# Kernel tuning notes

Hardware: AMD Instinct MI355X
Metric: run time of the kernel (lower is better)

## Reference

```python
import jax, jax.numpy as jnp
import numpy as np

D_MODEL = 1024
NHEAD = 16
HEAD_DIM = D_MODEL // NHEAD
ROPE_BASE = 10000.0


def rotate_half(x):
    h = x.shape[-1] // 2
    return jnp.concatenate((-x[..., h:], x[..., :h]), axis=-1)


def rope_cos_sin(seq_len, dim, dtype):
    inv_freq = 1.0 / (ROPE_BASE ** (jnp.arange(0, dim, 2, dtype=jnp.float32) / dim))
    t = jnp.arange(seq_len, dtype=jnp.float32)
    freqs = jnp.einsum('i,j->ij', t, inv_freq)  # [S, dim/2]
    emb = jnp.concatenate((freqs, freqs), axis=-1)  # [S, dim]
    return jnp.cos(emb).astype(dtype), jnp.sin(emb).astype(dtype)


def setup_inputs() -> dict:
    key = jax.random.key(0)
    ks = jax.random.split(key, 9)
    b, s = 2, 2048
    lim = 1.0 / np.sqrt(D_MODEL)
    def lin(kw, kb):
        W = jax.random.uniform(kw, (D_MODEL, D_MODEL), jnp.float32, -lim, lim)
        bia = jax.random.uniform(kb, (D_MODEL,), jnp.float32, -lim, lim)
        return W, bia
    Wq, bq = lin(ks[0], ks[1])
    Wk, bk = lin(ks[2], ks[3])
    Wv, bv = lin(ks[4], ks[5])
    Wo, bo = lin(ks[6], ks[7])
    x = jax.random.normal(ks[8], (b, s, D_MODEL), jnp.float32)
    return {"x": x, "Wq": Wq, "bq": bq, "Wk": Wk, "bk": bk,
            "Wv": Wv, "bv": bv, "Wo": Wo, "bo": bo}


def reference(x, Wq, bq, Wk, bk, Wv, bv, Wo, bo):
    b, s, _ = x.shape
    scale = jnp.sqrt(jnp.asarray(HEAD_DIM, x.dtype))
    # projections (torch Linear: y = x @ W.T + b)
    q = x @ Wq.T + bq
    k = x @ Wk.T + bk
    v = x @ Wv.T + bv
    # [b, h, s, d]
    def split_heads(t):
        return t.reshape(b, s, NHEAD, HEAD_DIM).transpose(0, 2, 1, 3)
    q, k, v = split_heads(q), split_heads(k), split_heads(v)
    cos, sin = rope_cos_sin(s, HEAD_DIM, x.dtype)  # [s, d]
    q = q * cos + rotate_half(q) * sin
    k = k * cos + rotate_half(k) * sin
    scores = jnp.einsum('bhqd,bhkd->bhqk', q, k) / scale
    probs = jax.nn.softmax(scores, axis=-1)
    out = jnp.einsum('bhqk,bhkd->bhqd', probs, v)
    out = out.transpose(0, 2, 1, 3).reshape(b, s, D_MODEL)
    return out @ Wo.T + bo
```

## Files before the change

kernel.cpp:

```cpp
#include <hip/hip_runtime.h>
#include <hip/hip_bf16.h>
#include <stdint.h>


typedef __attribute__((ext_vector_type(8))) short bf16x8;
typedef __attribute__((ext_vector_type(4))) float f32x4;
typedef __attribute__((ext_vector_type(16))) float f32x16;
typedef __attribute__((ext_vector_type(4))) short short4v;
typedef __attribute__((ext_vector_type(4))) float float4v;
typedef __attribute__((ext_vector_type(4))) unsigned uint32x4;

#define DEV __device__ __forceinline__

DEV short f2bf(float f) {
  union { float f; uint32_t u; } v; v.f = f;
  uint32_t r = (v.u + 0x7fffu + ((v.u >> 16) & 1u)) >> 16;
  return (short)(uint16_t)r;
}
DEV float bf2f(short b) {
  union { uint32_t u; float f; } v; v.u = ((uint32_t)(uint16_t)b) << 16;
  return v.f;
}
DEV unsigned cvtpk(float a, float b) {
  unsigned d;
  asm("v_cvt_pk_bf16_f32 %0, %1, %2" : "=v"(d) : "v"(a), "v"(b));
  return d;
}
DEV void gload16(const void* g, const void* l) {
  __builtin_amdgcn_global_load_lds((const __attribute__((address_space(1))) void*)g,
                                   (__attribute__((address_space(3))) void*)l, 16, 0, 0);
}

__global__ void convert_kernel(const float* __restrict__ x,
                               const float* __restrict__ wq, const float* __restrict__ wk,
                               const float* __restrict__ wv, const float* __restrict__ wo,
                               short* __restrict__ xb, short* __restrict__ wqb,
                               short* __restrict__ wkb, short* __restrict__ wvb,
                               short* __restrict__ wob,
                               float* __restrict__ ct, float* __restrict__ st) {
  const int idx = blockIdx.x * blockDim.x + threadIdx.x;
  if (idx >= 2097152) {
    const int i2 = idx - 2097152;
    const int t = i2 >> 5, j = i2 & 31;
    const float f = (float)t * exp2f(-(float)j * (13.287712379549449f / 32.f));
    ct[i2] = cosf(f);
    st[i2] = sinf(f);
    return;
  }
  const float* src; short* dst; int off;
  if (idx < 1048576)      { src = x;  dst = xb;  off = idx; }
  else if (idx < 1310720) { src = wq; dst = wqb; off = idx - 1048576; }
  else if (idx < 1572864) { src = wk; dst = wkb; off = idx - 1310720; }
  else if (idx < 1835008) { src = wv; dst = wvb; off = idx - 1572864; }
  else                    { src = wo; dst = wob; off = idx - 1835008; }
  float4v v = *(const float4v*)(src + (size_t)off * 4);
  short4v o;
  o[0] = f2bf(v[0]); o[1] = f2bf(v[1]); o[2] = f2bf(v[2]); o[3] = f2bf(v[3]);
  *(short4v*)(dst + (size_t)off * 4) = o;
}

template<bool FINAL>
__global__ __launch_bounds__(256, 2) void gemm_bt(
    const short* __restrict__ A,
    const short* __restrict__ W0, const short* __restrict__ W1, const short* __restrict__ W2,
    const float* __restrict__ b0, const float* __restrict__ b1, const float* __restrict__ b2,
    short* __restrict__ o0, short* __restrict__ o1, short* __restrict__ o2,
    float* __restrict__ of,
    const float* __restrict__ ct, const float* __restrict__ st) {
  constexpr int K = 1024;
  __shared__ short lds[2 * 128 * 64];
  short* As = lds;
  short* Ws = lds + 128 * 64;

  const int tid = threadIdx.x;
  const int lane = tid & 63;
  const int w = tid >> 6;
  const int wr = w >> 1, wc = w & 1;
  const int bn = blockIdx.x, bm = blockIdx.y, z = blockIdx.z;

  const short* Wt = (z == 0) ? W0 : (z == 1 ? W1 : W2);
  const float* bias = (z == 0) ? b0 : (z == 1 ? b1 : b2);
  short* ob = (z == 0) ? o0 : (z == 1 ? o1 : o2);

  const int lrow = lane >> 3;
  const int clog = 16 * ((lane & 7) ^ lrow);

  f32x4 acc[4][4] = {};
  const size_t arowbase = (size_t)(bm * 128) * K;
  const size_t wrowbase = (size_t)(bn * 128) * K;

  for (int kt = 0; kt < K / 64; ++kt) {
    __syncthreads();
#pragma unroll
    for (int i = 0; i < 4; ++i) {
      const int c = i * 4 + w;
      const int row = c * 8 + lrow;
      gload16(A + arowbase + (size_t)row * K + kt * 64 + (clog >> 1),
              (const char*)As + c * 1024);
      gload16(Wt + wrowbase + (size_t)row * K + kt * 64 + (clog >> 1),
              (const char*)Ws + c * 1024);
    }
    __syncthreads();
#pragma unroll
    for (int kk = 0; kk < 2; ++kk) {
      bf16x8 af[4], bf[4];
      const int kb = (kk * 32 + (lane >> 4) * 8) * 2;
#pragma unroll
      for (int mi = 0; mi < 4; ++mi) {
        const int row = wr * 64 + mi * 16 + (lane & 15);
        af[mi] = *(const bf16x8*)((const char*)As + row * 128 + (kb ^ ((row & 7) << 4)));
      }
#pragma unroll
      for (int ni = 0; ni < 4; ++ni) {
        const int row = wc * 64 + ni * 16 + (lane & 15);
        bf[ni] = *(const bf16x8*)((const char*)Ws + row * 128 + (kb ^ ((row & 7) << 4)));
      }
#pragma unroll
      for (int mi = 0; mi < 4; ++mi)
#pragma unroll
        for (int ni = 0; ni < 4; ++ni)
          acc[mi][ni] = __builtin_amdgcn_mfma_f32_16x16x32_bf16(af[mi], bf[ni], acc[mi][ni], 0, 0, 0);
    }
  }

  float bv[4];
#pragma unroll
  for (int ni = 0; ni < 4; ++ni)
    bv[ni] = bias[bn * 128 + wc * 64 + ni * 16 + (lane & 15)];

#pragma unroll
  for (int mi = 0; mi < 4; ++mi) {
#pragma unroll
    for (int r = 0; r < 4; ++r) {
      const int m = bm * 128 + wr * 64 + mi * 16 + (lane >> 4) * 4 + r;
      float v[4];
#pragma unroll
      for (int ni = 0; ni < 4; ++ni) v[ni] = acc[mi][ni][r] + bv[ni];
      if (!FINAL && z < 2) {
        const int s = m & 2047;
        const float sc = (z == 0) ? 0.18033688011f : 1.0f;
#pragma unroll
        for (int jj = 0; jj < 2; ++jj) {
          const int j = jj * 16 + (lane & 15);
          const float c = ct[s * 32 + j] * sc, sn = st[s * 32 + j] * sc;
          const float a = v[jj], bb = v[jj + 2];
          v[jj]     = a * c - bb * sn;
          v[jj + 2] = bb * c + a * sn;
        }
      }
#pragma unroll
      for (int ni = 0; ni < 4; ++ni) {
        const int n = bn * 128 + wc * 64 + ni * 16 + (lane & 15);
        if (FINAL) {
          of[(size_t)m * 1024 + n] = v[ni];
        } else {
          const int b = m >> 11, s = m & 2047, h = n >> 6, d = n & 63;
          ob[(((size_t)(b * 16 + h)) * 2048 + s) * 64 + d] = f2bf(v[ni]);
        }
      }
    }
  }
}

__global__ void vtrans_kernel(const short* __restrict__ v, short* __restrict__ vt) {
  __shared__ short t[64][72];
  const int bh = blockIdx.x, st0 = blockIdx.y * 64;
  const int tid = threadIdx.x;
#pragma unroll
  for (int i = 0; i < 2; ++i) {
    const int j = i * 256 + tid;
    const int row = j >> 3, c8 = (j & 7) * 8;
    *(bf16x8*)&t[row][c8] = *(const bf16x8*)(v + (((size_t)bh * 2048) + st0 + row) * 64 + c8);
  }
  __syncthreads();
#pragma unroll
  for (int i = 0; i < 2; ++i) {
    const int j = i * 256 + tid;
    const int dd = j >> 3, s8 = (j & 7) * 8;
    const int b16 = s8 & ~15;
    const int hi8 = (s8 >> 3) & 1;
    bf16x8 o;
#pragma unroll
    for (int e = 0; e < 8; ++e)
      o[e] = t[b16 + 4 * hi8 + (e & 3) + 8 * (e >> 2)][dd];
    *(bf16x8*)(vt + (((size_t)bh * 64) + dd) * 2048 + st0 + s8) = o;
  }
}

__global__ __launch_bounds__(256, 2) void attn_kernel(
    const short* __restrict__ q, const short* __restrict__ k,
    const short* __restrict__ vt, short* __restrict__ ao) {
  __shared__ char ldsb[65536];

  const int tid = threadIdx.x, lane = tid & 63, w = tid >> 6;
  const int wg = w & 1, g = w >> 1;
  const int hi = lane >> 5;
  const int bh = blockIdx.x, qt = blockIdx.y;
  const int lrow = lane >> 3;
  const int cshort = 8 * ((lane & 7) ^ lrow);

  const int qrow0 = qt * 128 + wg * 64 + (lane & 31);
  const short* qb = q + ((size_t)bh * 2048 + qrow0) * 64 + hi * 8;
  bf16x8 qf0[4], qf1[4];
#pragma unroll
  for (int m = 0; m < 4; ++m) {
    qf0[m] = *(const bf16x8*)(qb + 16 * m);
    qf1[m] = *(const bf16x8*)(qb + 32 * 64 + 16 * m);
  }

  f32x16 acc0[2] = {}, acc1[2] = {};
  float l0 = 0.f, l1 = 0.f;

  char* gbase = ldsb + g * 32768;
  const size_t kvoff = (size_t)g * 1024;

  const short* kp = k + ((size_t)bh * 2048 + kvoff + (wg * 4) * 8 + lrow) * 64 + cshort;
  const short* vp[4];
#pragma unroll
  for (int i = 0; i < 4; ++i)
    vp[i] = vt + ((size_t)bh * 64 + (wg * 4 + i) * 8 + lrow) * 2048 + kvoff + cshort;

#pragma unroll
  for (int i = 0; i < 4; ++i) {
    gload16(kp + i * 512, gbase + (wg * 4 + i) * 1024);
    gload16(vp[i], gbase + 8192 + (wg * 4 + i) * 1024);
  }
  kp += 4096;
#pragma unroll
  for (int i = 0; i < 4; ++i) vp[i] += 64;
  __syncthreads();

  int cur = 0;
  for (int j = 0; j < 16; ++j) {
    if (j < 15) {
      char* nb = gbase + (cur ^ 1) * 16384;
#pragma unroll
      for (int i = 0; i < 4; ++i) {
        gload16(kp + i * 512, nb + (wg * 4 + i) * 1024);
        gload16(vp[i], nb + 8192 + (wg * 4 + i) * 1024);
      }
      kp += 4096;
#pragma unroll
      for (int i = 0; i < 4; ++i) vp[i] += 64;
    }

    const char* kb_ = gbase + cur * 16384;
    const char* vb_ = kb_ + 8192;

    f32x16 stv0[2] = {}, stv1[2] = {};
#pragma unroll
    for (int t = 0; t < 2; ++t)
#pragma unroll
      for (int m = 0; m < 4; ++m) {
        const int bc = 32 * m + 16 * hi;
        const int row = t * 32 + (lane & 31);
        bf16x8 kf = *(const bf16x8*)(kb_ + row * 128 + (bc ^ ((row & 7) << 4)));
        stv0[t] = __builtin_amdgcn_mfma_f32_32x32x16_bf16(kf, qf0[m], stv0[t], 0, 0, 0);
        stv1[t] = __builtin_amdgcn_mfma_f32_32x32x16_bf16(kf, qf1[m], stv1[t], 0, 0, 0);
      }

#pragma unroll
    for (int t = 0; t < 2; ++t) {
#pragma unroll
      for (int r = 0; r < 16; ++r) {
        const float p0 = __builtin_amdgcn_exp2f(stv0[t][r]);
        const float p1 = __builtin_amdgcn_exp2f(stv1[t][r]);
        stv0[t][r] = p0; l0 += p0;
        stv1[t][r] = p1; l1 += p1;
      }
      uint32x4 pu0[2], pu1[2];
#pragma unroll
      for (int sl = 0; sl < 2; ++sl)
#pragma unroll
        for (int jj = 0; jj < 4; ++jj) {
          pu0[sl][jj] = cvtpk(stv0[t][8 * sl + 2 * jj], stv0[t][8 * sl + 2 * jj + 1]);
          pu1[sl][jj] = cvtpk(stv1[t][8 * sl + 2 * jj], stv1[t][8 * sl + 2 * jj + 1]);
        }
#pragma unroll
      for (int sl = 0; sl < 2; ++sl) {
        const bf16x8 pv0 = __builtin_bit_cast(bf16x8, pu0[sl]);
        const bf16x8 pv1 = __builtin_bit_cast(bf16x8, pu1[sl]);
        const int base = 64 * t + 32 * sl + 16 * hi;
#pragma unroll
        for (int db = 0; db < 2; ++db) {
          const int row = db * 32 + (lane & 31);
          const int sw = (row & 7) << 4;
          bf16x8 vv = *(const bf16x8*)(vb_ + row * 128 + (base ^ sw));
          acc0[db] = __builtin_amdgcn_mfma_f32_32x32x16_bf16(vv, pv0, acc0[db], 0, 0, 0);
          acc1[db] = __builtin_amdgcn_mfma_f32_32x32x16_bf16(vv, pv1, acc1[db], 0, 0, 0);
        }
      }
    }

    __syncthreads();
    cur ^= 1;
  }

  l0 += __shfl_xor(l0, 32);
  l1 += __shfl_xor(l1, 32);

  float* fm0 = (float*)(void*)ldsb + (wg * 2 + 0) * 2112;
  float* fm1 = (float*)(void*)ldsb + (wg * 2 + 1) * 2112;
  if (g == 1) {
    fm0[lane] = l0;
    fm1[lane] = l1;
#pragma unroll
    for (int db = 0; db < 2; ++db)
#pragma unroll
      for (int r = 0; r < 16; ++r) {
        fm0[64 + (db * 16 + r) * 64 + lane] = acc0[db][r];
        fm1[64 + (db * 16 + r) * 64 + lane] = acc1[db][r];
      }
  }
  __syncthreads();

  if (g == 0) {
    const int b = bh >> 4, h = bh & 15;
#pragma unroll
    for (int s = 0; s < 2; ++s) {
      float* fm = s ? fm1 : fm0;
      f32x16* accp = s ? acc1 : acc0;
      const float rl = 1.0f / ((s ? l1 : l0) + fm[lane]);
      const int qrow = qrow0 + 32 * s;
      short* orow = ao + ((size_t)b * 2048 + qrow) * 1024 + h * 64;
#pragma unroll
      for (int db = 0; db < 2; ++db)
#pragma unroll
        for (int gq = 0; gq < 4; ++gq) {
          short4v o;
#pragma unroll
          for (int jj = 0; jj < 4; ++jj) {
            const int r = 4 * gq + jj;
            const float v1 = fm[64 + (db * 16 + r) * 64 + lane];
            o[jj] = f2bf((accp[db][r] + v1) * rl);
          }
          *(short4v*)(orow + db * 32 + 8 * gq + 4 * hi) = o;
        }
    }
  }
}

extern "C" void kernel_launch(void* const* d_in, const int* in_sizes, int n_in,
                              void* d_out, int out_size, void* d_ws, size_t ws_size,
                              hipStream_t stream) {
  const float* x  = (const float*)d_in[0];
  const float* Wq = (const float*)d_in[1];
  const float* bq = (const float*)d_in[2];
  const float* Wk = (const float*)d_in[3];
  const float* bk = (const float*)d_in[4];
  const float* Wv = (const float*)d_in[5];
  const float* bv = (const float*)d_in[6];
  const float* Wo = (const float*)d_in[7];
  const float* bo = (const float*)d_in[8];
  float* out = (float*)d_out;

  char* ws = (char*)d_ws;
  short* xb  = (short*)(ws);
  short* wqb = (short*)(ws + 8388608);
  short* wkb = (short*)(ws + 10485760);
  short* wvb = (short*)(ws + 12582912);
  short* wob = (short*)(ws + 14680064);
  float* ct  = (float*)(ws + 16777216);
  float* st  = (float*)(ws + 17039360);
  short* qb  = (short*)(ws + 17301504);
  short* kb  = (short*)(ws + 25690112);
  short* vb  = (short*)(ws + 34078720);
  short* vtb = (short*)(ws + 42467328);
  short* ab  = (short*)(ws + 50855936);

  convert_kernel<<<dim3(8448), dim3(256), 0, stream>>>(
      x, Wq, Wk, Wv, Wo, xb, wqb, wkb, wvb, wob, ct, st);
  gemm_bt<false><<<dim3(8, 32, 3), dim3(256), 0, stream>>>(
      xb, wqb, wkb, wvb, bq, bk, bv, qb, kb, vb, (float*)nullptr, ct, st);
  vtrans_kernel<<<dim3(32, 32), dim3(256), 0, stream>>>(vb, vtb);
  attn_kernel<<<dim3(32, 16), dim3(256), 0, stream>>>(qb, kb, vtb, ab);
  gemm_bt<true><<<dim3(8, 32, 1), dim3(256), 0, stream>>>(
      ab, wob, (short*)nullptr, (short*)nullptr, bo, (float*)nullptr, (float*)nullptr,
      (short*)nullptr, (short*)nullptr, (short*)nullptr, out, ct, st);
}
```

Before: 106.2 us.

## Load K/V fragments directly from global memory instead of LDS double-buffer

```diff
diff --git a/kernel.cpp b/kernel.cpp
--- a/kernel.cpp
+++ b/kernel.cpp
@@ -190,14 +190,12 @@
 __global__ __launch_bounds__(256, 2) void attn_kernel(
     const short* __restrict__ q, const short* __restrict__ k,
     const short* __restrict__ vt, short* __restrict__ ao) {
-  __shared__ char ldsb[65536];
+  __shared__ float fm[4 * 2112];
 
   const int tid = threadIdx.x, lane = tid & 63, w = tid >> 6;
   const int wg = w & 1, g = w >> 1;
   const int hi = lane >> 5;
   const int bh = blockIdx.x, qt = blockIdx.y;
-  const int lrow = lane >> 3;
-  const int cshort = 8 * ((lane & 7) ^ lrow);
 
   const int qrow0 = qt * 128 + wg * 64 + (lane & 31);
   const short* qb = q + ((size_t)bh * 2048 + qrow0) * 64 + hi * 8;
@@ -211,50 +209,16 @@
   f32x16 acc0[2] = {}, acc1[2] = {};
   float l0 = 0.f, l1 = 0.f;
 
-  char* gbase = ldsb + g * 32768;
-  const size_t kvoff = (size_t)g * 1024;
-
-  const short* kp = k + ((size_t)bh * 2048 + kvoff + (wg * 4) * 8 + lrow) * 64 + cshort;
-  const short* vp[4];
-#pragma unroll
-  for (int i = 0; i < 4; ++i)
-    vp[i] = vt + ((size_t)bh * 64 + (wg * 4 + i) * 8 + lrow) * 2048 + kvoff + cshort;
-
-#pragma unroll
-  for (int i = 0; i < 4; ++i) {
-    gload16(kp + i * 512, gbase + (wg * 4 + i) * 1024);
-    gload16(vp[i], gbase + 8192 + (wg * 4 + i) * 1024);
-  }
-  kp += 4096;
-#pragma unroll
-  for (int i = 0; i < 4; ++i) vp[i] += 64;
-  __syncthreads();
-
-  int cur = 0;
+  const short* kp = k + ((size_t)bh * 2048 + g * 1024 + (lane & 31)) * 64 + 8 * hi;
+  const short* vp = vt + ((size_t)bh * 64 + (lane & 31)) * 2048 + g * 1024 + 8 * hi;
+
   for (int j = 0; j < 16; ++j) {
-    if (j < 15) {
-      char* nb = gbase + (cur ^ 1) * 16384;
-#pragma unroll
-      for (int i = 0; i < 4; ++i) {
-        gload16(kp + i * 512, nb + (wg * 4 + i) * 1024);
-        gload16(vp[i], nb + 8192 + (wg * 4 + i) * 1024);
-      }
-      kp += 4096;
-#pragma unroll
-      for (int i = 0; i < 4; ++i) vp[i] += 64;
-    }
-
-    const char* kb_ = gbase + cur * 16384;
-    const char* vb_ = kb_ + 8192;
-
     f32x16 stv0[2] = {}, stv1[2] = {};
 #pragma unroll
     for (int t = 0; t < 2; ++t)
 #pragma unroll
       for (int m = 0; m < 4; ++m) {
-        const int bc = 32 * m + 16 * hi;
-        const int row = t * 32 + (lane & 31);
-        bf16x8 kf = *(const bf16x8*)(kb_ + row * 128 + (bc ^ ((row & 7) << 4)));
+        bf16x8 kf = *(const bf16x8*)(kp + t * 2048 + 16 * m);
         stv0[t] = __builtin_amdgcn_mfma_f32_32x32x16_bf16(kf, qf0[m], stv0[t], 0, 0, 0);
         stv1[t] = __builtin_amdgcn_mfma_f32_32x32x16_bf16(kf, qf1[m], stv1[t], 0, 0, 0);
       }
@@ -280,27 +244,24 @@
       for (int sl = 0; sl < 2; ++sl) {
         const bf16x8 pv0 = __builtin_bit_cast(bf16x8, pu0[sl]);
         const bf16x8 pv1 = __builtin_bit_cast(bf16x8, pu1[sl]);
-        const int base = 64 * t + 32 * sl + 16 * hi;
 #pragma unroll
         for (int db = 0; db < 2; ++db) {
-          const int row = db * 32 + (lane & 31);
-          const int sw = (row & 7) << 4;
-          bf16x8 vv = *(const bf16x8*)(vb_ + row * 128 + (base ^ sw));
+          bf16x8 vv = *(const bf16x8*)(vp + db * 32 * 2048 + 32 * t + 16 * sl);
           acc0[db] = __builtin_amdgcn_mfma_f32_32x32x16_bf16(vv, pv0, acc0[db], 0, 0, 0);
           acc1[db] = __builtin_amdgcn_mfma_f32_32x32x16_bf16(vv, pv1, acc1[db], 0, 0, 0);
         }
       }
     }
 
-    __syncthreads();
-    cur ^= 1;
+    kp += 4096;
+    vp += 64;
   }
 
   l0 += __shfl_xor(l0, 32);
   l1 += __shfl_xor(l1, 32);
 
-  float* fm0 = (float*)(void*)ldsb + (wg * 2 + 0) * 2112;
-  float* fm1 = (float*)(void*)ldsb + (wg * 2 + 1) * 2112;
+  float* fm0 = fm + (wg * 2 + 0) * 2112;
+  float* fm1 = fm + (wg * 2 + 1) * 2112;
   if (g == 1) {
     fm0[lane] = l0;
     fm1[lane] = l1;
@@ -318,9 +279,9 @@
     const int b = bh >> 4, h = bh & 15;
 #pragma unroll
     for (int s = 0; s < 2; ++s) {
-      float* fm = s ? fm1 : fm0;
+      float* fmp = s ? fm1 : fm0;
       f32x16* accp = s ? acc1 : acc0;
-      const float rl = 1.0f / ((s ? l1 : l0) + fm[lane]);
+      const float rl = 1.0f / ((s ? l1 : l0) + fmp[lane]);
       const int qrow = qrow0 + 32 * s;
       short* orow = ao + ((size_t)b * 2048 + qrow) * 1024 + h * 64;
 #pragma unroll
@@ -331,7 +292,7 @@
 #pragma unroll
           for (int jj = 0; jj < 4; ++jj) {
             const int r = 4 * gq + jj;
-            const float v1 = fm[64 + (db * 16 + r) * 64 + lane];
+            const float v1 = fmp[64 + (db * 16 + r) * 64 + lane];
             o[jj] = f2bf((accp[db][r] + v1) * rl);
           }
           *(short4v*)(orow + db * 32 + 8 * gq + 4 * hi) = o;
```

After: 129.8 us. 22.3% more time.
